# Optimization experiments

Measured on AMD Instinct MI355X. Metric: run time of the kernel, lower is better.

Reference implementation:

```python
import jax, jax.numpy as jnp
import numpy as np

L = 128          # bandlimit
N_PHI = 2 * L - 1
BATCH, C_IN, C_OUT = 16, 8, 8


def _legendre_bar(L, theta):
    """Normalized associated Legendre P̄_l^m(cos theta) for m>=0.
    Returns [T, L, L] indexed [theta, l, m], zero for l < m.
    Normalization: Y_lm = P̄_l^m(cos th) e^{i m phi} (orthonormal on S^2).
    """
    T = theta.shape[0]
    x, s = np.cos(theta), np.sin(theta)
    P = np.zeros((T, L, L), dtype=np.float64)
    P[:, 0, 0] = np.sqrt(1.0 / (4.0 * np.pi))
    for m in range(1, L):
        P[:, m, m] = -np.sqrt((2.0 * m + 1.0) / (2.0 * m)) * s * P[:, m - 1, m - 1]
    for m in range(L):
        if m + 1 < L:
            P[:, m + 1, m] = np.sqrt(2.0 * m + 3.0) * x * P[:, m, m]
        for l in range(m + 2, L):
            a = np.sqrt((4.0 * l * l - 1.0) / (l * l - m * m))
            b = np.sqrt(((l - 1.0) ** 2 - m * m) / (4.0 * (l - 1.0) ** 2 - 1.0))
            P[:, l, m] = a * (x * P[:, l - 1, m] - b * P[:, l - 2, m])
    return P


def _transform_mats(L):
    """MW-sampled synthesis matrices Psyn[m, t, l] and their per-m
    pseudoinverse Pinv[m, l, t] (exact analysis on bandlimited signals)."""
    theta = np.pi * (2.0 * np.arange(L) + 1.0) / (2.0 * L - 1.0)  # MW theta grid
    Pbar = _legendre_bar(L, theta)                                # [T, L, L]
    ms = np.arange(-(L - 1), L)
    Psyn = np.zeros((2 * L - 1, L, L), dtype=np.float64)          # [m, t, l]
    for j, m in enumerate(ms):
        am = abs(m)
        sign = (-1.0) ** am if m < 0 else 1.0                     # P̄_l^{-m} = (-1)^m P̄_l^m
        Psyn[j] = sign * Pbar[:, :, am]
    Pinv = np.stack([np.linalg.pinv(Psyn[j]) for j in range(2 * L - 1)])  # [m, l, t]
    return Psyn.astype(np.float32), Pinv.astype(np.float32)


def sht(f, Pinv):
    """Forward spherical harmonic transform on MW grid. f: [..., T, 2L-1] real.
    Returns flm [..., L, 2L-1] complex (m ordered -(L-1)..L-1)."""
    nphi = f.shape[-1]
    F = jnp.fft.fftshift(jnp.fft.fft(f, axis=-1), axes=-1) / nphi  # [..., t, m]
    return jnp.einsum('...tm,mlt->...lm', F, Pinv)


def isht(flm, Psyn):
    """Inverse spherical harmonic transform. flm: [..., L, 2L-1] complex."""
    G = jnp.einsum('...lm,mtl->...tm', flm, Psyn)  # [..., t, m]
    nphi = G.shape[-1]
    return nphi * jnp.fft.ifft(jnp.fft.ifftshift(G, axes=-1), axis=-1)


def setup_inputs() -> dict:
    key = jax.random.key(0)
    k1, k2, k3 = jax.random.split(key, 3)
    x = jax.random.normal(k1, (BATCH, C_IN, L, N_PHI), dtype=jnp.float32)
    weight = jax.random.normal(k2, (C_OUT, C_IN, L, N_PHI), dtype=jnp.float32)
    bias = jax.random.normal(k3, (1, C_OUT, 1, 1), dtype=jnp.float32)
    Psyn, Pinv = _transform_mats(L)
    return {"x": x, "weight": weight, "bias": bias,
            "Psyn": jnp.asarray(Psyn), "Pinv": jnp.asarray(Pinv)}


def reference(x, weight, bias, Psyn, Pinv):
    # 1. transform kernel and signal to harmonic domain (batched, no host loops)
    w_lm = sht(weight, Pinv)                       # [O, I, L, M] complex64
    x_lm = sht(x, Pinv)                            # [B, I, L, M] complex64
    # 2. harmonic-domain multiply + channel contraction ('icl,oicl->ocl' per batch)
    out_lm = jnp.einsum('bilm,oilm->bolm', x_lm, w_lm)
    # 3. back to spatial domain (real part, as the original stores into a float tensor)
    out = jnp.real(isht(out_lm, Psyn)) + bias      # [B, O, L, 2L-1]
    return out
```

## Files before the change

### kernel.cpp

```cpp
#include <hip/hip_runtime.h>

#define PI_ 3.14159265358979323846

typedef __attribute__((ext_vector_type(8))) short bf16x8;
typedef __attribute__((ext_vector_type(4))) float f32x4;
typedef __attribute__((ext_vector_type(8))) unsigned short u16x8;
typedef unsigned short u16;

__device__ inline u16 f2bf(float f) {
  unsigned u = __float_as_uint(f);
  unsigned r = (u + 0x7FFFu + ((u >> 16) & 1u)) >> 16;
  return (u16)r;
}
__device__ inline float bf2f(u16 h) { return __uint_as_float(((unsigned)h) << 16); }
__device__ inline void splitf(float v, u16& h, u16& l) {
  h = f2bf(v);
  l = f2bf(v - bf2f(h));
}

__global__ void k_tab1(u16* __restrict__ B1h, u16* __restrict__ B1l) {
  int idx = blockIdx.x * 256 + threadIdx.x;
  if (idx >= 128 * 256) return;
  int n = idx >> 8, p = idx & 255;
  int j = n >> 1, kind = n & 1;
  double ang = (2.0 * PI_ / 255.0) * (double)(2 * j) * (double)p;
  double v = (p < 255) ? (kind ? -sin(ang) : cos(ang)) * (1.0 / 255.0) : 0.0;
  u16 h, l; splitf((float)v, h, l);
  B1h[idx] = h; B1l[idx] = l;
}
__global__ void k_tab2(u16* __restrict__ B5h, u16* __restrict__ B5l) {
  int idx = blockIdx.x * 256 + threadIdx.x;
  if (idx >= 256 * 128) return;
  int p = idx >> 7, k = idx & 127;
  int j = k >> 1, kind = k & 1;
  double ang = (2.0 * PI_ / 255.0) * (double)(2 * j) * (double)p;
  double sc = (j == 0) ? 1.0 : 2.0;
  double v = (p < 255) ? sc * (kind ? -sin(ang) : cos(ang)) : 0.0;
  u16 h, l; splitf((float)v, h, l);
  B5h[idx] = h; B5l[idx] = l;
}

#define MFMA __builtin_amdgcn_mfma_f32_16x16x32_bf16

__global__ __launch_bounds__(256) void k_s1(
    const float* __restrict__ x, const float* __restrict__ w,
    const u16* __restrict__ B1h, const u16* __restrict__ B1l,
    u16* __restrict__ Xh, u16* __restrict__ Xl) {
  const int u0 = blockIdx.x * 64;
  const int n0 = blockIdx.y * 64;
  const int tid = threadIdx.x;
  const int sr = tid >> 2, sc = tid & 3;
  const int lane = tid & 63, wid = tid >> 6;
  const int wm = wid & 1, wn = wid >> 1;
  const int frow = lane & 15, fkg = lane >> 4;
  __shared__ u16 lds[4][2560];
  f32x4 acc[2][2] = {};
  const int u = u0 + sr;
  const float* src = (u < 16384) ? (x + (size_t)u * 255)
                                 : (w + (size_t)(u - 16384) * 255);
  for (int k0 = 0; k0 < 256; k0 += 32) {
    __syncthreads();
    {
      int kb = k0 + sc * 8;
      bf16x8 hv, lv;
      #pragma unroll
      for (int i = 0; i < 8; ++i) {
        int k = kb + i;
        float v = (k < 255) ? src[k] : 0.f;
        u16 h, l; splitf(v, h, l);
        hv[i] = (short)h; lv[i] = (short)l;
      }
      *reinterpret_cast<bf16x8*>(&lds[0][sr * 40 + sc * 8]) = hv;
      *reinterpret_cast<bf16x8*>(&lds[1][sr * 40 + sc * 8]) = lv;
    }
    {
      size_t o = (size_t)(n0 + sr) * 256 + k0 + sc * 8;
      *reinterpret_cast<bf16x8*>(&lds[2][sr * 40 + sc * 8]) =
          *reinterpret_cast<const bf16x8*>(&B1h[o]);
      *reinterpret_cast<bf16x8*>(&lds[3][sr * 40 + sc * 8]) =
          *reinterpret_cast<const bf16x8*>(&B1l[o]);
    }
    __syncthreads();
    bf16x8 ah[2], al[2], bh[2], bl[2];
    #pragma unroll
    for (int fm = 0; fm < 2; ++fm) {
      int ar = wm * 32 + fm * 16 + frow;
      ah[fm] = *reinterpret_cast<const bf16x8*>(&lds[0][ar * 40 + fkg * 8]);
      al[fm] = *reinterpret_cast<const bf16x8*>(&lds[1][ar * 40 + fkg * 8]);
    }
    #pragma unroll
    for (int fn = 0; fn < 2; ++fn) {
      int br = wn * 32 + fn * 16 + frow;
      bh[fn] = *reinterpret_cast<const bf16x8*>(&lds[2][br * 40 + fkg * 8]);
      bl[fn] = *reinterpret_cast<const bf16x8*>(&lds[3][br * 40 + fkg * 8]);
    }
    #pragma unroll
    for (int fn = 0; fn < 2; ++fn)
      #pragma unroll
      for (int fm = 0; fm < 2; ++fm) {
        acc[fm][fn] = MFMA(ah[fm], bh[fn], acc[fm][fn], 0, 0, 0);
        acc[fm][fn] = MFMA(ah[fm], bl[fn], acc[fm][fn], 0, 0, 0);
        acc[fm][fn] = MFMA(al[fm], bh[fn], acc[fm][fn], 0, 0, 0);
      }
  }
  #pragma unroll
  for (int fm = 0; fm < 2; ++fm)
    #pragma unroll
    for (int fn = 0; fn < 2; ++fn) {
      int gm = u0 + wm * 32 + fm * 16 + fkg * 4;
      int gn = n0 + wn * 32 + fn * 16 + frow;
      int j = gn >> 1, kind = gn & 1;
      int rp = (gm < 16384) ? (gm >> 7) : (128 + ((gm - 16384) >> 7));
      int tb = gm & 127;
      u16 h[4], l[4];
      #pragma unroll
      for (int r = 0; r < 4; ++r) splitf(acc[fm][fn][r], h[r], l[r]);
      size_t o = ((size_t)(j * 2 + kind) * 192 + rp) * 128 + tb;
      *reinterpret_cast<ushort4*>(&Xh[o]) = make_ushort4(h[0], h[1], h[2], h[3]);
      *reinterpret_cast<ushort4*>(&Xl[o]) = make_ushort4(l[0], l[1], l[2], l[3]);
    }
}

__global__ __launch_bounds__(256) void k_s2(
    const u16* __restrict__ Xh, const u16* __restrict__ Xl,
    const float* __restrict__ Pinv,
    u16* __restrict__ XLh, u16* __restrict__ XLl) {
  const int j = blockIdx.x;
  const int l0 = (blockIdx.y & 1) * 64;
  const int nt = blockIdx.y >> 1;
  const int kind = (nt >= 3) ? 1 : 0;
  const int rp0 = (nt - 3 * kind) * 64;
  const int tid = threadIdx.x;
  const int sr = tid >> 2, sc = tid & 3;
  const int lane = tid & 63, wid = tid >> 6;
  const int wm = wid & 1, wn = wid >> 1;
  const int frow = lane & 15, fkg = lane >> 4;
  __shared__ u16 lds[4][2560];
  f32x4 acc[2][2] = {};
  const int m = 127 + 2 * j;
  const float* asrc = Pinv + ((size_t)m * 128 + l0 + sr) * 128;
  const u16* bbase_h = Xh + ((size_t)(j * 2 + kind) * 192 + rp0 + sr) * 128;
  const u16* bbase_l = Xl + ((size_t)(j * 2 + kind) * 192 + rp0 + sr) * 128;
  for (int k0 = 0; k0 < 128; k0 += 32) {
    __syncthreads();
    {
      const float4* ap = reinterpret_cast<const float4*>(asrc + k0 + sc * 8);
      float4 v0 = ap[0], v1 = ap[1];
      float vv[8] = {v0.x, v0.y, v0.z, v0.w, v1.x, v1.y, v1.z, v1.w};
      bf16x8 hv, lv;
      #pragma unroll
      for (int i = 0; i < 8; ++i) { u16 h, l; splitf(vv[i], h, l); hv[i] = (short)h; lv[i] = (short)l; }
      *reinterpret_cast<bf16x8*>(&lds[0][sr * 40 + sc * 8]) = hv;
      *reinterpret_cast<bf16x8*>(&lds[1][sr * 40 + sc * 8]) = lv;
    }
    {
      *reinterpret_cast<bf16x8*>(&lds[2][sr * 40 + sc * 8]) =
          *reinterpret_cast<const bf16x8*>(&bbase_h[k0 + sc * 8]);
      *reinterpret_cast<bf16x8*>(&lds[3][sr * 40 + sc * 8]) =
          *reinterpret_cast<const bf16x8*>(&bbase_l[k0 + sc * 8]);
    }
    __syncthreads();
    bf16x8 ah[2], al[2], bh[2], bl[2];
    #pragma unroll
    for (int fm = 0; fm < 2; ++fm) {
      int ar = wm * 32 + fm * 16 + frow;
      ah[fm] = *reinterpret_cast<const bf16x8*>(&lds[0][ar * 40 + fkg * 8]);
      al[fm] = *reinterpret_cast<const bf16x8*>(&lds[1][ar * 40 + fkg * 8]);
    }
    #pragma unroll
    for (int fn = 0; fn < 2; ++fn) {
      int br = wn * 32 + fn * 16 + frow;
      bh[fn] = *reinterpret_cast<const bf16x8*>(&lds[2][br * 40 + fkg * 8]);
      bl[fn] = *reinterpret_cast<const bf16x8*>(&lds[3][br * 40 + fkg * 8]);
    }
    #pragma unroll
    for (int fn = 0; fn < 2; ++fn)
      #pragma unroll
      for (int fm = 0; fm < 2; ++fm) {
        acc[fm][fn] = MFMA(ah[fm], bh[fn], acc[fm][fn], 0, 0, 0);
        acc[fm][fn] = MFMA(ah[fm], bl[fn], acc[fm][fn], 0, 0, 0);
        acc[fm][fn] = MFMA(al[fm], bh[fn], acc[fm][fn], 0, 0, 0);
      }
  }
  #pragma unroll
  for (int fm = 0; fm < 2; ++fm)
    #pragma unroll
    for (int fn = 0; fn < 2; ++fn) {
      int l = l0 + wm * 32 + fm * 16 + fkg * 4;
      int rp = rp0 + wn * 32 + fn * 16 + frow;
      u16 h[4], lo[4];
      #pragma unroll
      for (int r = 0; r < 4; ++r) splitf(acc[fm][fn][r], h[r], lo[r]);
      size_t o = ((size_t)(j * 2 + kind) * 192 + rp) * 128 + l;
      *reinterpret_cast<ushort4*>(&XLh[o]) = make_ushort4(h[0], h[1], h[2], h[3]);
      *reinterpret_cast<ushort4*>(&XLl[o]) = make_ushort4(lo[0], lo[1], lo[2], lo[3]);
    }
}

__global__ __launch_bounds__(256) void k_s3(
    const u16* __restrict__ XLh, const u16* __restrict__ XLl,
    u16* __restrict__ OLh, u16* __restrict__ OLl) {
  const int j = blockIdx.x;
  const int l0 = blockIdx.y * 16;
  const int tid = threadIdx.x;
  __shared__ float Xs[2][128][17];
  __shared__ float Ws[2][64][17];
  for (int idx = tid; idx < 2 * 192 * 16; idx += 256) {
    int kind = idx / (192 * 16);
    int rem = idx - kind * (192 * 16);
    int rp = rem >> 4, lc = rem & 15;
    size_t src = ((size_t)(j * 2 + kind) * 192 + rp) * 128 + l0 + lc;
    float v = bf2f(XLh[src]) + bf2f(XLl[src]);
    if (rp < 128) Xs[kind][rp][lc] = v; else Ws[kind][rp - 128][lc] = v;
  }
  __syncthreads();
  const int bo = tid & 127, lg = tid >> 7;
  const int b = bo >> 3, o = bo & 7;
  u16 hr[8], lr[8], hi[8], li[8];
  #pragma unroll
  for (int i2 = 0; i2 < 8; ++i2) {
    int lc = lg * 8 + i2;
    float ar = 0.f, ai = 0.f;
    #pragma unroll
    for (int i = 0; i < 8; ++i) {
      float xr = Xs[0][b * 8 + i][lc], xi = Xs[1][b * 8 + i][lc];
      float wr = Ws[0][o * 8 + i][lc], wi = Ws[1][o * 8 + i][lc];
      ar += xr * wr - xi * wi;
      ai += xr * wi + xi * wr;
    }
    splitf(ar, hr[i2], lr[i2]);
    splitf(ai, hi[i2], li[i2]);
  }
  size_t o0 = ((size_t)(j * 2 + 0) * 128 + bo) * 128 + l0 + lg * 8;
  size_t o1 = ((size_t)(j * 2 + 1) * 128 + bo) * 128 + l0 + lg * 8;
  u16x8 v;
  #pragma unroll
  for (int i = 0; i < 8; ++i) v[i] = hr[i];
  *reinterpret_cast<u16x8*>(&OLh[o0]) = v;
  #pragma unroll
  for (int i = 0; i < 8; ++i) v[i] = lr[i];
  *reinterpret_cast<u16x8*>(&OLl[o0]) = v;
  #pragma unroll
  for (int i = 0; i < 8; ++i) v[i] = hi[i];
  *reinterpret_cast<u16x8*>(&OLh[o1]) = v;
  #pragma unroll
  for (int i = 0; i < 8; ++i) v[i] = li[i];
  *reinterpret_cast<u16x8*>(&OLl[o1]) = v;
}

__global__ __launch_bounds__(256) void k_s4(
    const u16* __restrict__ OLh, const u16* __restrict__ OLl,
    const float* __restrict__ Psyn,
    u16* __restrict__ Gh, u16* __restrict__ Gl) {
  const int j = blockIdx.x;
  const int t0 = (blockIdx.y & 1) * 64;
  const int nt = blockIdx.y >> 1;
  const int kind = nt >> 1;
  const int bo0 = (nt & 1) * 64;
  const int tid = threadIdx.x;
  const int sr = tid >> 2, sc = tid & 3;
  const int lane = tid & 63, wid = tid >> 6;
  const int wm = wid & 1, wn = wid >> 1;
  const int frow = lane & 15, fkg = lane >> 4;
  __shared__ u16 lds[4][2560];
  f32x4 acc[2][2] = {};
  const int m = 127 + 2 * j;
  const float* asrc = Psyn + ((size_t)m * 128 + t0 + sr) * 128;
  const u16* bbase_h = OLh + ((size_t)(j * 2 + kind) * 128 + bo0 + sr) * 128;
  const u16* bbase_l = OLl + ((size_t)(j * 2 + kind) * 128 + bo0 + sr) * 128;
  for (int k0 = 0; k0 < 128; k0 += 32) {
    __syncthreads();
    {
      const float4* ap = reinterpret_cast<const float4*>(asrc + k0 + sc * 8);
      float4 v0 = ap[0], v1 = ap[1];
      float vv[8] = {v0.x, v0.y, v0.z, v0.w, v1.x, v1.y, v1.z, v1.w};
      bf16x8 hv, lv;
      #pragma unroll
      for (int i = 0; i < 8; ++i) { u16 h, l; splitf(vv[i], h, l); hv[i] = (short)h; lv[i] = (short)l; }
      *reinterpret_cast<bf16x8*>(&lds[0][sr * 40 + sc * 8]) = hv;
      *reinterpret_cast<bf16x8*>(&lds[1][sr * 40 + sc * 8]) = lv;
    }
    {
      *reinterpret_cast<bf16x8*>(&lds[2][sr * 40 + sc * 8]) =
          *reinterpret_cast<const bf16x8*>(&bbase_h[k0 + sc * 8]);
      *reinterpret_cast<bf16x8*>(&lds[3][sr * 40 + sc * 8]) =
          *reinterpret_cast<const bf16x8*>(&bbase_l[k0 + sc * 8]);
    }
    __syncthreads();
    bf16x8 ah[2], al[2], bh[2], bl[2];
    #pragma unroll
    for (int fm = 0; fm < 2; ++fm) {
      int ar = wm * 32 + fm * 16 + frow;
      ah[fm] = *reinterpret_cast<const bf16x8*>(&lds[0][ar * 40 + fkg * 8]);
      al[fm] = *reinterpret_cast<const bf16x8*>(&lds[1][ar * 40 + fkg * 8]);
    }
    #pragma unroll
    for (int fn = 0; fn < 2; ++fn) {
      int br = wn * 32 + fn * 16 + frow;
      bh[fn] = *reinterpret_cast<const bf16x8*>(&lds[2][br * 40 + fkg * 8]);
      bl[fn] = *reinterpret_cast<const bf16x8*>(&lds[3][br * 40 + fkg * 8]);
    }
    #pragma unroll
    for (int fn = 0; fn < 2; ++fn)
      #pragma unroll
      for (int fm = 0; fm < 2; ++fm) {
        acc[fm][fn] = MFMA(ah[fm], bh[fn], acc[fm][fn], 0, 0, 0);
        acc[fm][fn] = MFMA(ah[fm], bl[fn], acc[fm][fn], 0, 0, 0);
        acc[fm][fn] = MFMA(al[fm], bh[fn], acc[fm][fn], 0, 0, 0);
      }
  }
  #pragma unroll
  for (int fm = 0; fm < 2; ++fm)
    #pragma unroll
    for (int fn = 0; fn < 2; ++fn) {
      int tt = t0 + wm * 32 + fm * 16 + fkg * 4;
      int bo = bo0 + wn * 32 + fn * 16 + frow;
      #pragma unroll
      for (int r = 0; r < 4; ++r) {
        u16 h, l; splitf(acc[fm][fn][r], h, l);
        size_t o = ((size_t)bo * 128 + tt + r) * 128 + 2 * j + kind;
        Gh[o] = h; Gl[o] = l;
      }
    }
}

__global__ __launch_bounds__(256) void k_s5(
    const u16* __restrict__ Gh, const u16* __restrict__ Gl,
    const u16* __restrict__ B5h, const u16* __restrict__ B5l,
    const float* __restrict__ bias, float* __restrict__ out) {
  const int u0 = blockIdx.x * 64;
  const int p0 = blockIdx.y * 64;
  const int tid = threadIdx.x;
  const int sr = tid >> 2, sc = tid & 3;
  const int lane = tid & 63, wid = tid >> 6;
  const int wm = wid & 1, wn = wid >> 1;
  const int frow = lane & 15, fkg = lane >> 4;
  __shared__ u16 lds[4][2560];
  f32x4 acc[2][2] = {};
  const u16* abase_h = Gh + (size_t)(u0 + sr) * 128;
  const u16* abase_l = Gl + (size_t)(u0 + sr) * 128;
  const u16* bbase_h = B5h + (size_t)(p0 + sr) * 128;
  const u16* bbase_l = B5l + (size_t)(p0 + sr) * 128;
  for (int k0 = 0; k0 < 128; k0 += 32) {
    __syncthreads();
    *reinterpret_cast<bf16x8*>(&lds[0][sr * 40 + sc * 8]) =
        *reinterpret_cast<const bf16x8*>(&abase_h[k0 + sc * 8]);
    *reinterpret_cast<bf16x8*>(&lds[1][sr * 40 + sc * 8]) =
        *reinterpret_cast<const bf16x8*>(&abase_l[k0 + sc * 8]);
    *reinterpret_cast<bf16x8*>(&lds[2][sr * 40 + sc * 8]) =
        *reinterpret_cast<const bf16x8*>(&bbase_h[k0 + sc * 8]);
    *reinterpret_cast<bf16x8*>(&lds[3][sr * 40 + sc * 8]) =
        *reinterpret_cast<const bf16x8*>(&bbase_l[k0 + sc * 8]);
    __syncthreads();
    bf16x8 ah[2], al[2], bh[2], bl[2];
    #pragma unroll
    for (int fm = 0; fm < 2; ++fm) {
      int ar = wm * 32 + fm * 16 + frow;
      ah[fm] = *reinterpret_cast<const bf16x8*>(&lds[0][ar * 40 + fkg * 8]);
      al[fm] = *reinterpret_cast<const bf16x8*>(&lds[1][ar * 40 + fkg * 8]);
    }
    #pragma unroll
    for (int fn = 0; fn < 2; ++fn) {
      int br = wn * 32 + fn * 16 + frow;
      bh[fn] = *reinterpret_cast<const bf16x8*>(&lds[2][br * 40 + fkg * 8]);
      bl[fn] = *reinterpret_cast<const bf16x8*>(&lds[3][br * 40 + fkg * 8]);
    }
    #pragma unroll
    for (int fn = 0; fn < 2; ++fn)
      #pragma unroll
      for (int fm = 0; fm < 2; ++fm) {
        acc[fm][fn] = MFMA(ah[fm], bh[fn], acc[fm][fn], 0, 0, 0);
        acc[fm][fn] = MFMA(ah[fm], bl[fn], acc[fm][fn], 0, 0, 0);
        acc[fm][fn] = MFMA(al[fm], bh[fn], acc[fm][fn], 0, 0, 0);
      }
  }
  const int bo = u0 >> 7;
  const float bv = bias[bo & 7];
  #pragma unroll
  for (int fm = 0; fm < 2; ++fm)
    #pragma unroll
    for (int fn = 0; fn < 2; ++fn) {
      int u5 = u0 + wm * 32 + fm * 16 + fkg * 4;
      int p = p0 + wn * 32 + fn * 16 + frow;
      int t = u5 & 127;
      if (p < 255) {
        #pragma unroll
        for (int r = 0; r < 4; ++r)
          out[((size_t)bo * 128 + t + r) * 255 + p] = acc[fm][fn][r] + bv;
      }
    }
}

extern "C" void kernel_launch(void* const* d_in, const int* in_sizes, int n_in,
                              void* d_out, int out_size, void* d_ws, size_t ws_size,
                              hipStream_t stream) {
  const float* x    = (const float*)d_in[0];
  const float* w    = (const float*)d_in[1];
  const float* bias = (const float*)d_in[2];
  const float* Psyn = (const float*)d_in[3];
  const float* Pinv = (const float*)d_in[4];
  float* out = (float*)d_out;

  u16* ws = (u16*)d_ws;
  const size_t PLX = 3145728;
  u16* Xh  = ws;
  u16* Xl  = ws + PLX;
  u16* XLh = ws + 2 * PLX;
  u16* XLl = ws + 3 * PLX;
  u16* B1h = XLh;
  u16* B1l = XLh + 32768;
  u16* OLh = Xh;
  u16* OLl = Xl;
  u16* B5h = Xh + 2097152;
  u16* B5l = Xl + 2097152;
  u16* Gh = XLh;
  u16* Gl = XLl;

  k_tab1<<<128, 256, 0, stream>>>(B1h, B1l);
  k_s1<<<dim3(384, 2), 256, 0, stream>>>(x, w, B1h, B1l, Xh, Xl);
  k_s2<<<dim3(64, 12), 256, 0, stream>>>(Xh, Xl, Pinv, XLh, XLl);
  k_tab2<<<128, 256, 0, stream>>>(B5h, B5l);
  k_s3<<<dim3(64, 8), 256, 0, stream>>>(XLh, XLl, OLh, OLl);
  k_s4<<<dim3(64, 8), 256, 0, stream>>>(OLh, OLl, Psyn, Gh, Gl);
  k_s5<<<dim3(256, 4), 256, 0, stream>>>(Gh, Gl, B5h, B5l, bias, out);
}
```

Baseline: 181.0 us.

## Transpose G intermediate layout for coalesced stores and merge twiddle-table kernels

The s4 epilogue now writes G in a [k][bo][t] layout using 4-wide vector stores, where it used to do scattered 2-byte stores strided by 128 elements. The s5 A-tile load reads this layout with 16-byte vector loads and transposes it into LDS with scalar 2-byte writes. The two DFT table kernels are merged into one launch, and the workspace is rearranged so the tables no longer alias the intermediates. The aim is to remove uncoalesced global writes and one kernel launch, at the cost of possible LDS bank conflicts in the scalar transpose writes.

New measurement: 158.2 us. 1.14x faster.

```diff
diff --git a/kernel.cpp b/kernel.cpp
--- a/kernel.cpp
+++ b/kernel.cpp
@@ -18,26 +18,27 @@
   l = f2bf(v - bf2f(h));
 }
 
-__global__ void k_tab1(u16* __restrict__ B1h, u16* __restrict__ B1l) {
+__global__ void k_tab(u16* __restrict__ B1h, u16* __restrict__ B1l,
+                      u16* __restrict__ B5h, u16* __restrict__ B5l) {
   int idx = blockIdx.x * 256 + threadIdx.x;
-  if (idx >= 128 * 256) return;
-  int n = idx >> 8, p = idx & 255;
-  int j = n >> 1, kind = n & 1;
-  double ang = (2.0 * PI_ / 255.0) * (double)(2 * j) * (double)p;
-  double v = (p < 255) ? (kind ? -sin(ang) : cos(ang)) * (1.0 / 255.0) : 0.0;
-  u16 h, l; splitf((float)v, h, l);
-  B1h[idx] = h; B1l[idx] = l;
-}
-__global__ void k_tab2(u16* __restrict__ B5h, u16* __restrict__ B5l) {
-  int idx = blockIdx.x * 256 + threadIdx.x;
-  if (idx >= 256 * 128) return;
-  int p = idx >> 7, k = idx & 127;
-  int j = k >> 1, kind = k & 1;
-  double ang = (2.0 * PI_ / 255.0) * (double)(2 * j) * (double)p;
-  double sc = (j == 0) ? 1.0 : 2.0;
-  double v = (p < 255) ? sc * (kind ? -sin(ang) : cos(ang)) : 0.0;
-  u16 h, l; splitf((float)v, h, l);
-  B5h[idx] = h; B5l[idx] = l;
+  if (idx < 128 * 256) {
+    int n = idx >> 8, p = idx & 255;
+    int j = n >> 1, kind = n & 1;
+    double ang = (2.0 * PI_ / 255.0) * (double)(2 * j) * (double)p;
+    double v = (p < 255) ? (kind ? -sin(ang) : cos(ang)) * (1.0 / 255.0) : 0.0;
+    u16 h, l; splitf((float)v, h, l);
+    B1h[idx] = h; B1l[idx] = l;
+  } else {
+    int i2 = idx - 128 * 256;
+    if (i2 >= 256 * 128) return;
+    int p = i2 >> 7, k = i2 & 127;
+    int j = k >> 1, kind = k & 1;
+    double ang = (2.0 * PI_ / 255.0) * (double)(2 * j) * (double)p;
+    double sc = (j == 0) ? 1.0 : 2.0;
+    double v = (p < 255) ? sc * (kind ? -sin(ang) : cos(ang)) : 0.0;
+    u16 h, l; splitf((float)v, h, l);
+    B5h[i2] = h; B5l[i2] = l;
+  }
 }
 
 #define MFMA __builtin_amdgcn_mfma_f32_16x16x32_bf16
@@ -315,12 +316,12 @@
     for (int fn = 0; fn < 2; ++fn) {
       int tt = t0 + wm * 32 + fm * 16 + fkg * 4;
       int bo = bo0 + wn * 32 + fn * 16 + frow;
-      #pragma unroll
-      for (int r = 0; r < 4; ++r) {
-        u16 h, l; splitf(acc[fm][fn][r], h, l);
-        size_t o = ((size_t)bo * 128 + tt + r) * 128 + 2 * j + kind;
-        Gh[o] = h; Gl[o] = l;
-      }
+      u16 h[4], l[4];
+      #pragma unroll
+      for (int r = 0; r < 4; ++r) splitf(acc[fm][fn][r], h[r], l[r]);
+      size_t o = ((size_t)(2 * j + kind) * 128 + bo) * 128 + tt;
+      *reinterpret_cast<ushort4*>(&Gh[o]) = make_ushort4(h[0], h[1], h[2], h[3]);
+      *reinterpret_cast<ushort4*>(&Gl[o]) = make_ushort4(l[0], l[1], l[2], l[3]);
     }
 }
 
@@ -330,27 +331,37 @@
     const float* __restrict__ bias, float* __restrict__ out) {
   const int u0 = blockIdx.x * 64;
   const int p0 = blockIdx.y * 64;
+  const int bo = u0 >> 7;
+  const int t0 = u0 & 127;
   const int tid = threadIdx.x;
   const int sr = tid >> 2, sc = tid & 3;
+  const int kk = tid >> 3;
+  const int tb8 = (tid & 7) * 8;
   const int lane = tid & 63, wid = tid >> 6;
   const int wm = wid & 1, wn = wid >> 1;
   const int frow = lane & 15, fkg = lane >> 4;
   __shared__ u16 lds[4][2560];
   f32x4 acc[2][2] = {};
-  const u16* abase_h = Gh + (size_t)(u0 + sr) * 128;
-  const u16* abase_l = Gl + (size_t)(u0 + sr) * 128;
   const u16* bbase_h = B5h + (size_t)(p0 + sr) * 128;
   const u16* bbase_l = B5l + (size_t)(p0 + sr) * 128;
   for (int k0 = 0; k0 < 128; k0 += 32) {
     __syncthreads();
-    *reinterpret_cast<bf16x8*>(&lds[0][sr * 40 + sc * 8]) =
-        *reinterpret_cast<const bf16x8*>(&abase_h[k0 + sc * 8]);
-    *reinterpret_cast<bf16x8*>(&lds[1][sr * 40 + sc * 8]) =
-        *reinterpret_cast<const bf16x8*>(&abase_l[k0 + sc * 8]);
-    *reinterpret_cast<bf16x8*>(&lds[2][sr * 40 + sc * 8]) =
-        *reinterpret_cast<const bf16x8*>(&bbase_h[k0 + sc * 8]);
-    *reinterpret_cast<bf16x8*>(&lds[3][sr * 40 + sc * 8]) =
-        *reinterpret_cast<const bf16x8*>(&bbase_l[k0 + sc * 8]);
+    {
+      size_t src = ((size_t)(k0 + kk) * 128 + bo) * 128 + t0 + tb8;
+      bf16x8 hv = *reinterpret_cast<const bf16x8*>(&Gh[src]);
+      bf16x8 lv = *reinterpret_cast<const bf16x8*>(&Gl[src]);
+      #pragma unroll
+      for (int i = 0; i < 8; ++i) {
+        lds[0][(tb8 + i) * 40 + kk] = (u16)(unsigned short)hv[i];
+        lds[1][(tb8 + i) * 40 + kk] = (u16)(unsigned short)lv[i];
+      }
+    }
+    {
+      *reinterpret_cast<bf16x8*>(&lds[2][sr * 40 + sc * 8]) =
+          *reinterpret_cast<const bf16x8*>(&bbase_h[k0 + sc * 8]);
+      *reinterpret_cast<bf16x8*>(&lds[3][sr * 40 + sc * 8]) =
+          *reinterpret_cast<const bf16x8*>(&bbase_l[k0 + sc * 8]);
+    }
     __syncthreads();
     bf16x8 ah[2], al[2], bh[2], bl[2];
     #pragma unroll
@@ -374,7 +385,6 @@
         acc[fm][fn] = MFMA(al[fm], bh[fn], acc[fm][fn], 0, 0, 0);
       }
   }
-  const int bo = u0 >> 7;
   const float bv = bias[bo & 7];
   #pragma unroll
   for (int fm = 0; fm < 2; ++fm)
@@ -402,24 +412,24 @@
   float* out = (float*)d_out;
 
   u16* ws = (u16*)d_ws;
+  u16* B1h = ws;
+  u16* B1l = ws + 32768;
+  u16* B5h = ws + 2 * 32768;
+  u16* B5l = ws + 3 * 32768;
+  u16* base = ws + 4 * 32768;
   const size_t PLX = 3145728;
-  u16* Xh  = ws;
-  u16* Xl  = ws + PLX;
-  u16* XLh = ws + 2 * PLX;
-  u16* XLl = ws + 3 * PLX;
-  u16* B1h = XLh;
-  u16* B1l = XLh + 32768;
+  u16* Xh  = base;
+  u16* Xl  = base + PLX;
+  u16* XLh = base + 2 * PLX;
+  u16* XLl = base + 3 * PLX;
   u16* OLh = Xh;
   u16* OLl = Xl;
-  u16* B5h = Xh + 2097152;
-  u16* B5l = Xl + 2097152;
   u16* Gh = XLh;
   u16* Gl = XLl;
 
-  k_tab1<<<128, 256, 0, stream>>>(B1h, B1l);
+  k_tab<<<256, 256, 0, stream>>>(B1h, B1l, B5h, B5l);
   k_s1<<<dim3(384, 2), 256, 0, stream>>>(x, w, B1h, B1l, Xh, Xl);
   k_s2<<<dim3(64, 12), 256, 0, stream>>>(Xh, Xl, Pinv, XLh, XLl);
-  k_tab2<<<128, 256, 0, stream>>>(B5h, B5l);
   k_s3<<<dim3(64, 8), 256, 0, stream>>>(XLh, XLl, OLh, OLl);
   k_s4<<<dim3(64, 8), 256, 0, stream>>>(OLh, OLl, Psyn, Gh, Gl);
   k_s5<<<dim3(256, 4), 256, 0, stream>>>(Gh, Gl, B5h, B5l, bias, out);
```
